# Kernel tuning notes

Hardware: AMD Instinct MI355X
Metric: run time of the kernel (lower is better)

Reference implementation:

```python
import jax, jax.numpy as jnp
import numpy as np

D_MODEL = 512
NUM_EXPERTS = 8
TOP_K = 2
FFN = 2048
H = 2 * D_MODEL            # GRU hidden per direction
GRU_OUT = 4 * D_MODEL      # bidirectional concat
B, T = 8, 1024
BAL_W, Z_W = 0.01, 0.001


def setup_inputs() -> dict:
    key = jax.random.key(0)
    ks = jax.random.split(key, 12)
    s = 1.0 / np.sqrt(H)  # torch GRU uniform init scale
    u = lambda k, shape: jax.random.uniform(k, shape, jnp.float32, -s, s)
    tn = lambda k, shape: jax.random.normal(k, shape, jnp.float32) * 0.02
    return {
        "x": jax.random.normal(ks[0], (B, T, D_MODEL), jnp.float32),
        # GRU params, stacked [2 directions, ...]; gate order (r, z, n) as in torch
        "gru_Wih": u(ks[1], (2, 3 * H, D_MODEL)),
        "gru_Whh": u(ks[2], (2, 3 * H, H)),
        "gru_bih": u(ks[3], (2, 3 * H)),
        "gru_bhh": u(ks[4], (2, 3 * H)),
        "gate_W": tn(ks[5], (NUM_EXPERTS, GRU_OUT)),
        "gate_b": jnp.zeros((NUM_EXPERTS,), jnp.float32),
        "W1": tn(ks[6], (NUM_EXPERTS, GRU_OUT, FFN)),
        "b1": jnp.zeros((NUM_EXPERTS, FFN), jnp.float32),
        "W2": tn(ks[7], (NUM_EXPERTS, FFN, D_MODEL)),
        "b2": jnp.zeros((NUM_EXPERTS, D_MODEL), jnp.float32),
    }


def _gru_bidir(x, Wih, Whh, bih, bhh):
    # x: [B,T,D]; returns [B,T,2H]
    Bn = x.shape[0]

    def run(d, reverse):
        # precompute input projections: [T,B,3H]
        xg = jnp.swapaxes(jnp.einsum('btd,gd->btg', x, Wih[d]) + bih[d], 0, 1)
        Whh_d, bhh_d = Whh[d], bhh[d]

        def step(h, xt):
            hg = h @ Whh_d.T + bhh_d
            xr, xz, xn = jnp.split(xt, 3, axis=-1)
            hr, hz, hn = jnp.split(hg, 3, axis=-1)
            r = jax.nn.sigmoid(xr + hr)
            z = jax.nn.sigmoid(xz + hz)
            n = jnp.tanh(xn + r * hn)
            h_new = (1.0 - z) * n + z * h
            return h_new, h_new

        h0 = jnp.zeros((Bn, H), x.dtype)
        _, ys = jax.lax.scan(step, h0, xg, reverse=reverse)  # ys[t] aligned with time t
        return jnp.swapaxes(ys, 0, 1)

    return jnp.concatenate([run(0, False), run(1, True)], axis=-1)


def reference(x, gru_Wih, gru_Whh, gru_bih, gru_bhh, gate_W, gate_b, W1, b1, W2, b2):
    Bn, Tn, _ = x.shape
    n = Bn * Tn
    E = NUM_EXPERTS

    gru_out = _gru_bidir(x, gru_Wih, gru_Whh, gru_bih, gru_bhh)
    gru_out = jax.nn.leaky_relu(gru_out, 0.01)          # dropout=0.0 -> identity
    flat = gru_out.reshape(n, GRU_OUT)

    # gating (expert_bias buffer is zeros at init)
    logits = flat @ gate_W.T + gate_b                    # [n,E]
    z_loss = Z_W * jnp.mean(jnp.square(jax.nn.logsumexp(logits, axis=-1)))
    scores = jax.nn.softmax(logits, axis=-1)
    top_scores, top_idx = jax.lax.top_k(scores, TOP_K)   # [n,K]
    weights = top_scores / jnp.sum(top_scores, axis=-1, keepdims=True)

    expert_mask = jnp.sum(jax.nn.one_hot(top_idx, E, dtype=jnp.float32), axis=1)  # [n,E]
    f = jax.lax.stop_gradient(jnp.mean(expert_mask, axis=0))
    P = jnp.mean(scores, axis=0)
    balance_loss = BAL_W * E * jnp.sum(f * P)
    aux_loss = balance_loss + z_loss

    # masked-dense expert combine (math identical to gather/scatter loop)
    output = jnp.zeros((n, D_MODEL), jnp.float32)
    for e in range(E):
        h = jax.nn.gelu(flat @ W1[e] + b1[e], approximate=False)  # [n,FFN]
        out_e = h @ W2[e] + b2[e]                                 # [n,D]
        w_e = jnp.sum(weights * (top_idx == e), axis=-1)          # [n]
        output = output + w_e[:, None] * out_e

    return output.reshape(Bn, Tn, D_MODEL).astype(x.dtype), aux_loss
```

## Files before the change

### kernel.cpp

```cpp
#include <hip/hip_runtime.h>
#include <math.h>

#define NTOK 8192
#define DM   512
#define HID  1024
#define G3H  3072
#define GOUT 2048
#define FFND 2048
#define NEXP 8

typedef float f32x4 __attribute__((ext_vector_type(4)));

#define XG_OFF    0ULL
#define HG_OFF    0ULL
#define OG_OFF    134217728ULL
#define FLAT_OFF  201326592ULL
#define HBUF_OFF  268435456ULL
#define FLAGS_OFF 268566528ULL
#define IMETA_OFF 268567552ULL
#define FMETA_OFF 268571648ULL
#define TKIDX_OFF 268575744ULL
#define TKW_OFF   268641280ULL
#define PAIRT_OFF 268706816ULL
#define PAIRW_OFF 268772352ULL
#define SLOT_OFF  268837888ULL

__global__ void k0_init(float* p) {
    int i = blockIdx.x * 256 + threadIdx.x;
    if (i < 35072) p[i] = 0.f;
}

__global__ __launch_bounds__(256, 2) void k1_sgemm_bt(
    const float* __restrict__ A, const float* __restrict__ B,
    const float* __restrict__ bias, float* __restrict__ C) {
    __shared__ float As[16 * 132];
    __shared__ float Bs[16 * 132];
    const int tid = threadIdx.x;
    const int m0 = blockIdx.y * 128;
    const int n0 = blockIdx.x * 128;
    const int tx = tid & 15, ty = tid >> 4;
    const int arow = tid >> 2, ac4 = (tid & 3) * 4;
    float acc[8][8];
#pragma unroll
    for (int i = 0; i < 8; ++i)
#pragma unroll
        for (int j = 0; j < 8; ++j) acc[i][j] = 0.f;

    for (int k0 = 0; k0 < 512; k0 += 16) {
        __syncthreads();
#pragma unroll
        for (int r = 0; r < 2; ++r) {
            int row = r * 64 + arow;
            float4 va = *(const float4*)(A + (size_t)(m0 + row) * 512 + k0 + ac4);
            As[(ac4 + 0) * 132 + row] = va.x;
            As[(ac4 + 1) * 132 + row] = va.y;
            As[(ac4 + 2) * 132 + row] = va.z;
            As[(ac4 + 3) * 132 + row] = va.w;
            float4 vb = *(const float4*)(B + (size_t)(n0 + row) * 512 + k0 + ac4);
            Bs[(ac4 + 0) * 132 + row] = vb.x;
            Bs[(ac4 + 1) * 132 + row] = vb.y;
            Bs[(ac4 + 2) * 132 + row] = vb.z;
            Bs[(ac4 + 3) * 132 + row] = vb.w;
        }
        __syncthreads();
#pragma unroll
        for (int k = 0; k < 16; ++k) {
            float4 a0 = *(const float4*)&As[k * 132 + ty * 8];
            float4 a1 = *(const float4*)&As[k * 132 + ty * 8 + 4];
            float4 b0 = *(const float4*)&Bs[k * 132 + tx * 8];
            float4 b1 = *(const float4*)&Bs[k * 132 + tx * 8 + 4];
            float av[8] = {a0.x, a0.y, a0.z, a0.w, a1.x, a1.y, a1.z, a1.w};
            float bv[8] = {b0.x, b0.y, b0.z, b0.w, b1.x, b1.y, b1.z, b1.w};
#pragma unroll
            for (int i = 0; i < 8; ++i)
#pragma unroll
                for (int j = 0; j < 8; ++j) acc[i][j] = fmaf(av[i], bv[j], acc[i][j]);
        }
    }
    float4 c0 = *(const float4*)(bias + n0 + tx * 8);
    float4 c1 = *(const float4*)(bias + n0 + tx * 8 + 4);
    float bb[8] = {c0.x, c0.y, c0.z, c0.w, c1.x, c1.y, c1.z, c1.w};
#pragma unroll
    for (int i = 0; i < 8; ++i) {
        float* op = C + (size_t)(m0 + ty * 8 + i) * 6144 + n0 + tx * 8;
        float4 o0 = make_float4(acc[i][0] + bb[0], acc[i][1] + bb[1],
                                acc[i][2] + bb[2], acc[i][3] + bb[3]);
        float4 o1 = make_float4(acc[i][4] + bb[4], acc[i][5] + bb[5],
                                acc[i][6] + bb[6], acc[i][7] + bb[7]);
        *(float4*)op = o0;
        *(float4*)(op + 4) = o1;
    }
}

__global__ __launch_bounds__(256) void k2_gru(
    const float* __restrict__ Whh, const float* __restrict__ bhh,
    const float* __restrict__ xg, float* __restrict__ flat,
    float* hbuf, int* flags) {
    __shared__ float hlsf[8192];
    __shared__ float red[64 * 196];
    __shared__ float s2b[192];
    char* hls = (char*)hlsf;
    const int tid = threadIdx.x;
    const int dir = blockIdx.x >> 7;
    const int wg = blockIdx.x & 127;
    const int j0 = wg << 3;
    float* hb = hbuf + dir * 16384;
    int* fl = flags + dir * 128;
    const int rg = tid >> 6;
    const int kc = tid & 63;
    const int swz = (kc & 7) << 4;
    const int lane = tid & 63;

    const float* W0 = Whh + (size_t)dir * G3H * HID;
    float wreg[6][16];
#pragma unroll
    for (int rr = 0; rr < 6; ++rr) {
        const int r = rg * 6 + rr;
        const float* wp = W0 + (size_t)(((r >> 3) << 10) + j0 + (r & 7)) * 1024 + (kc << 4);
        const float4 w0 = ((const float4*)wp)[0];
        const float4 w1 = ((const float4*)wp)[1];
        const float4 w2 = ((const float4*)wp)[2];
        const float4 w3 = ((const float4*)wp)[3];
        wreg[rr][0] = w0.x;  wreg[rr][1] = w0.y;  wreg[rr][2] = w0.z;  wreg[rr][3] = w0.w;
        wreg[rr][4] = w1.x;  wreg[rr][5] = w1.y;  wreg[rr][6] = w1.z;  wreg[rr][7] = w1.w;
        wreg[rr][8] = w2.x;  wreg[rr][9] = w2.y;  wreg[rr][10] = w2.z; wreg[rr][11] = w2.w;
        wreg[rr][12] = w3.x; wreg[rr][13] = w3.y; wreg[rr][14] = w3.z; wreg[rr][15] = w3.w;
    }
    float bhh_r = 0.f;
    if (tid < 192) {
        const int r = tid >> 3;
        bhh_r = bhh[dir * G3H + ((r >> 3) << 10) + j0 + (r & 7)];
    }
    const int u = tid >> 3, bb = tid & 7;
    const int wswz = ((tid >> 5) & 7) << 4;
    float hprev = 0.f;

    for (int s = 1; s <= 1024; ++s) {
        const int te = dir ? (1024 - s) : (s - 1);
        float xr = 0.f, xz = 0.f, xn = 0.f;
        if (tid < 64) {
            const float* xp = xg + (size_t)((bb << 10) + te) * 6144 + dir * G3H + j0 + u;
            xr = xp[0];
            xz = xp[1024];
            xn = xp[2048];
        }
        if (s > 1) {
            const int c0 = s - 1;
            int it = 0;
            for (;;) {
                int f0 = __hip_atomic_load(fl + lane, __ATOMIC_RELAXED, __HIP_MEMORY_SCOPE_AGENT);
                int f1 = __hip_atomic_load(fl + 64 + lane, __ATOMIC_RELAXED, __HIP_MEMORY_SCOPE_AGENT);
                if (__all((f0 >= c0) && (f1 >= c0))) break;
                if (++it > (1 << 22)) break;
                __builtin_amdgcn_s_sleep(1);
            }
        }
        asm volatile("" ::: "memory");
        const float* hp = hb + (((s - 1) & 1) << 13);
        const float* hbase = hp + (tid << 2);
        f32x4 hv4[8];
#pragma unroll
        for (int c = 0; c < 8; ++c)
            asm volatile("global_load_dwordx4 %0, %1, off sc0 sc1"
                         : "=v"(hv4[c]) : "v"(hbase + (c << 10)));
        asm volatile("s_waitcnt vmcnt(0)" ::: "memory");
        __builtin_amdgcn_sched_barrier(0);
#pragma unroll
        for (int c = 0; c < 8; ++c) {
            const int off = ((c << 12) + (tid << 4)) ^ wswz;
            *(f32x4*)(hls + off) = hv4[c];
        }
        __syncthreads();
        float acc[6][8];
#pragma unroll
        for (int rr = 0; rr < 6; ++rr)
#pragma unroll
            for (int q = 0; q < 8; ++q) acc[rr][q] = 0.f;
#pragma unroll
        for (int i = 0; i < 16; ++i) {
            const int kbase = ((kc << 4) + i) << 5;
            const float4 hA = *(const float4*)(hls + (kbase ^ swz));
            const float4 hB = *(const float4*)(hls + ((kbase + 16) ^ swz));
#pragma unroll
            for (int rr = 0; rr < 6; ++rr) {
                const float w = wreg[rr][i];
                acc[rr][0] = fmaf(w, hA.x, acc[rr][0]);
                acc[rr][1] = fmaf(w, hA.y, acc[rr][1]);
                acc[rr][2] = fmaf(w, hA.z, acc[rr][2]);
                acc[rr][3] = fmaf(w, hA.w, acc[rr][3]);
                acc[rr][4] = fmaf(w, hB.x, acc[rr][4]);
                acc[rr][5] = fmaf(w, hB.y, acc[rr][5]);
                acc[rr][6] = fmaf(w, hB.z, acc[rr][6]);
                acc[rr][7] = fmaf(w, hB.w, acc[rr][7]);
            }
        }
        float* rp = red + kc * 196 + rg * 48;
#pragma unroll
        for (int rr = 0; rr < 6; ++rr) {
            *(float4*)(rp + (rr << 3)) =
                make_float4(acc[rr][0], acc[rr][1], acc[rr][2], acc[rr][3]);
            *(float4*)(rp + (rr << 3) + 4) =
                make_float4(acc[rr][4], acc[rr][5], acc[rr][6], acc[rr][7]);
        }
        __syncthreads();
        if (tid < 192) {
            float a0 = 0.f, a1 = 0.f, a2 = 0.f, a3 = 0.f;
#pragma unroll
            for (int q = 0; q < 64; q += 4) {
                a0 += red[(q + 0) * 196 + tid];
                a1 += red[(q + 1) * 196 + tid];
                a2 += red[(q + 2) * 196 + tid];
                a3 += red[(q + 3) * 196 + tid];
            }
            s2b[tid] = (a0 + a1) + (a2 + a3) + bhh_r;
        }
        __syncthreads();
        if (tid < 64) {
            const float hr = s2b[tid];
            const float hz = s2b[64 + tid];
            const float hn = s2b[128 + tid];
            const float rg_ = 1.f / (1.f + expf(-(xr + hr)));
            const float zg_ = 1.f / (1.f + expf(-(xz + hz)));
            const float ng_ = tanhf(xn + rg_ * hn);
            const float hnew = (1.f - zg_) * ng_ + zg_ * hprev;
            hprev = hnew;
            __hip_atomic_store(hb + ((s & 1) << 13) + ((j0 + u) << 3) + bb, hnew,
                               __ATOMIC_RELAXED, __HIP_MEMORY_SCOPE_AGENT);
            __builtin_amdgcn_s_waitcnt(0);
            if (tid == 0)
                __hip_atomic_store(fl + wg, s, __ATOMIC_RELAXED, __HIP_MEMORY_SCOPE_AGENT);
            const float lr = hnew > 0.f ? hnew : 0.01f * hnew;
            flat[(size_t)((bb << 10) + te) * 2048 + dir * 1024 + j0 + u] = lr;
        }
    }
}

__global__ __launch_bounds__(256) void k3_gate(
    const float* __restrict__ flat, const float* __restrict__ gate_W,
    const float* __restrict__ gate_b,
    int* __restrict__ tk_idx, float* __restrict__ tk_w,
    int* __restrict__ counts, float* __restrict__ fmeta) {
    __shared__ float gw[8 * 2048];
    __shared__ float bP[9];
    __shared__ int bC[8];
    const int tid = threadIdx.x;
    for (int i = tid; i < 8 * 2048; i += 256) gw[i] = gate_W[i];
    if (tid < 9) bP[tid] = 0.f;
    if (tid < 8) bC[tid] = 0;
    __syncthreads();
    const int lane = tid & 63, w = tid >> 6;
    const int tbase = blockIdx.x * 16 + w * 4;
    for (int j = 0; j < 4; ++j) {
        int t = tbase + j;
        const float* fr = flat + (size_t)t * 2048;
        float a[8];
#pragma unroll
        for (int e = 0; e < 8; ++e) a[e] = 0.f;
        for (int i = 0; i < 32; ++i) {
            float v = fr[i * 64 + lane];
#pragma unroll
            for (int e = 0; e < 8; ++e) a[e] = fmaf(v, gw[e * 2048 + i * 64 + lane], a[e]);
        }
#pragma unroll
        for (int e = 0; e < 8; ++e) {
#pragma unroll
            for (int off = 32; off > 0; off >>= 1) a[e] += __shfl_down(a[e], off);
        }
        if (lane == 0) {
            float lg[8];
#pragma unroll
            for (int e = 0; e < 8; ++e) lg[e] = a[e] + gate_b[e];
            float m = lg[0];
#pragma unroll
            for (int e = 1; e < 8; ++e) m = fmaxf(m, lg[e]);
            float sc[8], ssum = 0.f;
#pragma unroll
            for (int e = 0; e < 8; ++e) { sc[e] = expf(lg[e] - m); ssum += sc[e]; }
            float inv = 1.f / ssum;
#pragma unroll
            for (int e = 0; e < 8; ++e) sc[e] *= inv;
            float lse = m + logf(ssum);
            int i1 = 0; float s1 = sc[0];
#pragma unroll
            for (int e = 1; e < 8; ++e) if (sc[e] > s1) { s1 = sc[e]; i1 = e; }
            int i2 = (i1 == 0) ? 1 : 0; float s2v = sc[i2];
#pragma unroll
            for (int e = 0; e < 8; ++e) if (e != i1 && sc[e] > s2v) { s2v = sc[e]; i2 = e; }
            float wsum = s1 + s2v;
            tk_idx[2 * t] = i1; tk_idx[2 * t + 1] = i2;
            tk_w[2 * t] = s1 / wsum; tk_w[2 * t + 1] = s2v / wsum;
            atomicAdd(&bC[i1], 1);
            atomicAdd(&bC[i2], 1);
#pragma unroll
            for (int e = 0; e < 8; ++e) atomicAdd(&bP[e], sc[e]);
            atomicAdd(&bP[8], lse * lse);
        }
    }
    __syncthreads();
    if (tid < 8) {
        atomicAdd(&counts[tid], bC[tid]);
        atomicAdd(&fmeta[tid], bP[tid]);
    }
    if (tid == 8) atomicAdd(&fmeta[8], bP[8]);
}

__global__ void k4_sched(int* im, float* fm, float* aux_out) {
    int tid = threadIdx.x;
    if (tid < 136) { im[32 + tid] = -1; im[168 + tid] = 0; }
    __syncthreads();
    if (tid == 0) {
        int off = 0;
        for (int e = 0; e < 8; ++e) { im[16 + e] = off; im[8 + e] = off; off += im[e]; }
        im[24] = off;
        int T = 0;
        for (int e = 0; e < 8; ++e) {
            int c = im[e], o = im[16 + e];
            for (int i = 0; i < c; i += 128) { im[32 + T] = e; im[168 + T] = o + i; ++T; }
        }
        im[25] = T;
        float fP = 0.f;
        for (int e = 0; e < 8; ++e) fP += ((float)im[e] / 8192.f) * (fm[e] / 8192.f);
        *aux_out = 0.01f * 8.f * fP + 0.001f * (fm[8] / 8192.f);
    }
}

__global__ __launch_bounds__(256) void k5_scatter(
    const int* __restrict__ tk_idx, const float* __restrict__ tk_w,
    int* __restrict__ im, int* __restrict__ pair_t,
    float* __restrict__ pair_w, int* __restrict__ slot) {
    __shared__ int cnt[8], base[8];
    const int tid = threadIdx.x;
    if (tid < 8) cnt[tid] = 0;
    __syncthreads();
    const int t = blockIdx.x * 256 + tid;
    const int e0 = tk_idx[2 * t], e1 = tk_idx[2 * t + 1];
    const int p0 = atomicAdd(&cnt[e0], 1);
    const int p1 = atomicAdd(&cnt[e1], 1);
    __syncthreads();
    if (tid < 8) base[tid] = atomicAdd(&im[8 + tid], cnt[tid]);
    __syncthreads();
    const int q0 = base[e0] + p0, q1 = base[e1] + p1;
    pair_t[q0] = t; pair_w[q0] = tk_w[2 * t];     slot[2 * t] = q0;
    pair_t[q1] = t; pair_w[q1] = tk_w[2 * t + 1]; slot[2 * t + 1] = q1;
}

__global__ __launch_bounds__(256, 2) void k6_ffn1(
    const float* __restrict__ flat, const float* __restrict__ W1,
    const float* __restrict__ b1, const int* __restrict__ im,
    const int* __restrict__ pair_t, float* __restrict__ Hg) {
    const int rt = blockIdx.x % 136;
    const int nt = blockIdx.x / 136;
    const int e = im[32 + rt];
    if (e < 0) return;
    const int pStart = im[168 + rt];
    const int pEnd = im[16 + e + 1];
    __shared__ float As[16 * 132];
    __shared__ float Bs[16 * 132];
    const int tid = threadIdx.x;
    const int tx = tid & 15, ty = tid >> 4;
    const int n0 = nt * 128;
    const float* Bb = W1 + (size_t)e * 2048 * 2048;
    const int arow = tid >> 2, ac4 = (tid & 3) * 4;
    const int bk = tid >> 4, bn = (tid & 15) * 8;
    int r0 = pStart + arow;       if (r0 > pEnd - 1) r0 = pEnd - 1;
    int r1 = pStart + 64 + arow;  if (r1 > pEnd - 1) r1 = pEnd - 1;
    const float* arp0 = flat + (size_t)pair_t[r0] * 2048;
    const float* arp1 = flat + (size_t)pair_t[r1] * 2048;
    float acc[8][8];
#pragma unroll
    for (int i = 0; i < 8; ++i)
#pragma unroll
        for (int j = 0; j < 8; ++j) acc[i][j] = 0.f;

    for (int k0 = 0; k0 < 2048; k0 += 16) {
        __syncthreads();
        {
            float4 va = *(const float4*)(arp0 + k0 + ac4);
            As[(ac4 + 0) * 132 + arow] = va.x;
            As[(ac4 + 1) * 132 + arow] = va.y;
            As[(ac4 + 2) * 132 + arow] = va.z;
            As[(ac4 + 3) * 132 + arow] = va.w;
            float4 vb = *(const float4*)(arp1 + k0 + ac4);
            As[(ac4 + 0) * 132 + 64 + arow] = vb.x;
            As[(ac4 + 1) * 132 + 64 + arow] = vb.y;
            As[(ac4 + 2) * 132 + 64 + arow] = vb.z;
            As[(ac4 + 3) * 132 + 64 + arow] = vb.w;
            float4 w0 = *(const float4*)(Bb + (size_t)(k0 + bk) * 2048 + n0 + bn);
            float4 w1 = *(const float4*)(Bb + (size_t)(k0 + bk) * 2048 + n0 + bn + 4);
            *(float4*)&Bs[bk * 132 + bn] = w0;
            *(float4*)&Bs[bk * 132 + bn + 4] = w1;
        }
        __syncthreads();
#pragma unroll
        for (int k = 0; k < 16; ++k) {
            float4 a0 = *(const float4*)&As[k * 132 + ty * 8];
            float4 a1 = *(const float4*)&As[k * 132 + ty * 8 + 4];
            float4 b0 = *(const float4*)&Bs[k * 132 + tx * 8];
            float4 b1v = *(const float4*)&Bs[k * 132 + tx * 8 + 4];
            float av[8] = {a0.x, a0.y, a0.z, a0.w, a1.x, a1.y, a1.z, a1.w};
            float bv[8] = {b0.x, b0.y, b0.z, b0.w, b1v.x, b1v.y, b1v.z, b1v.w};
#pragma unroll
            for (int i = 0; i < 8; ++i)
#pragma unroll
                for (int j = 0; j < 8; ++j) acc[i][j] = fmaf(av[i], bv[j], acc[i][j]);
        }
    }
    float4 c0 = *(const float4*)(b1 + (size_t)e * 2048 + n0 + tx * 8);
    float4 c1 = *(const float4*)(b1 + (size_t)e * 2048 + n0 + tx * 8 + 4);
    float bb[8] = {c0.x, c0.y, c0.z, c0.w, c1.x, c1.y, c1.z, c1.w};
#pragma unroll
    for (int i = 0; i < 8; ++i) {
        int p = pStart + ty * 8 + i;
        if (p < pEnd) {
            float* op = Hg + (size_t)p * 2048 + n0 + tx * 8;
            float o[8];
#pragma unroll
            for (int j = 0; j < 8; ++j) {
                float xv = acc[i][j] + bb[j];
                o[j] = 0.5f * xv * (1.f + erff(xv * 0.70710678118654752f));
            }
            *(float4*)op = make_float4(o[0], o[1], o[2], o[3]);
            *(float4*)(op + 4) = make_float4(o[4], o[5], o[6], o[7]);
        }
    }
}

__global__ __launch_bounds__(256, 2) void k7_ffn2(
    const float* __restrict__ Hg, const float* __restrict__ W2,
    const float* __restrict__ b2, const int* __restrict__ im,
    float* __restrict__ Og) {
    const int rt = blockIdx.x % 136;
    const int nt = blockIdx.x / 136;
    const int e = im[32 + rt];
    if (e < 0) return;
    const int pStart = im[168 + rt];
    const int pEnd = im[16 + e + 1];
    __shared__ float As[16 * 132];
    __shared__ float Bs[16 * 132];
    const int tid = threadIdx.x;
    const int tx = tid & 15, ty = tid >> 4;
    const int n0 = nt * 128;
    const float* Bb = W2 + (size_t)e * 2048 * 512;
    const int arow = tid >> 2, ac4 = (tid & 3) * 4;
    const int bk = tid >> 4, bn = (tid & 15) * 8;
    int r0 = pStart + arow;       if (r0 > pEnd - 1) r0 = pEnd - 1;
    int r1 = pStart + 64 + arow;  if (r1 > pEnd - 1) r1 = pEnd - 1;
    const float* arp0 = Hg + (size_t)r0 * 2048;
    const float* arp1 = Hg + (size_t)r1 * 2048;
    float acc[8][8];
#pragma unroll
    for (int i = 0; i < 8; ++i)
#pragma unroll
        for (int j = 0; j < 8; ++j) acc[i][j] = 0.f;

    for (int k0 = 0; k0 < 2048; k0 += 16) {
        __syncthreads();
        {
            float4 va = *(const float4*)(arp0 + k0 + ac4);
            As[(ac4 + 0) * 132 + arow] = va.x;
            As[(ac4 + 1) * 132 + arow] = va.y;
            As[(ac4 + 2) * 132 + arow] = va.z;
            As[(ac4 + 3) * 132 + arow] = va.w;
            float4 vb = *(const float4*)(arp1 + k0 + ac4);
            As[(ac4 + 0) * 132 + 64 + arow] = vb.x;
            As[(ac4 + 1) * 132 + 64 + arow] = vb.y;
            As[(ac4 + 2) * 132 + 64 + arow] = vb.z;
            As[(ac4 + 3) * 132 + 64 + arow] = vb.w;
            float4 w0 = *(const float4*)(Bb + (size_t)(k0 + bk) * 512 + n0 + bn);
            float4 w1 = *(const float4*)(Bb + (size_t)(k0 + bk) * 512 + n0 + bn + 4);
            *(float4*)&Bs[bk * 132 + bn] = w0;
            *(float4*)&Bs[bk * 132 + bn + 4] = w1;
        }
        __syncthreads();
#pragma unroll
        for (int k = 0; k < 16; ++k) {
            float4 a0 = *(const float4*)&As[k * 132 + ty * 8];
            float4 a1 = *(const float4*)&As[k * 132 + ty * 8 + 4];
            float4 b0 = *(const float4*)&Bs[k * 132 + tx * 8];
            float4 b1v = *(const float4*)&Bs[k * 132 + tx * 8 + 4];
            float av[8] = {a0.x, a0.y, a0.z, a0.w, a1.x, a1.y, a1.z, a1.w};
            float bv[8] = {b0.x, b0.y, b0.z, b0.w, b1v.x, b1v.y, b1v.z, b1v.w};
#pragma unroll
            for (int i = 0; i < 8; ++i)
#pragma unroll
                for (int j = 0; j < 8; ++j) acc[i][j] = fmaf(av[i], bv[j], acc[i][j]);
        }
    }
    float4 c0 = *(const float4*)(b2 + (size_t)e * 512 + n0 + tx * 8);
    float4 c1 = *(const float4*)(b2 + (size_t)e * 512 + n0 + tx * 8 + 4);
    float bb[8] = {c0.x, c0.y, c0.z, c0.w, c1.x, c1.y, c1.z, c1.w};
#pragma unroll
    for (int i = 0; i < 8; ++i) {
        int p = pStart + ty * 8 + i;
        if (p < pEnd) {
            float* op = Og + (size_t)p * 512 + n0 + tx * 8;
            *(float4*)op = make_float4(acc[i][0] + bb[0], acc[i][1] + bb[1],
                                       acc[i][2] + bb[2], acc[i][3] + bb[3]);
            *(float4*)(op + 4) = make_float4(acc[i][4] + bb[4], acc[i][5] + bb[5],
                                             acc[i][6] + bb[6], acc[i][7] + bb[7]);
        }
    }
}

__global__ __launch_bounds__(256) void k8_comb(
    const float* __restrict__ Og, const int* __restrict__ slot,
    const float* __restrict__ pw, float* __restrict__ out) {
    const int i4 = blockIdx.x * 256 + threadIdx.x;
    const int t = i4 >> 7;
    const int d = (i4 & 127) << 2;
    const int s0 = slot[2 * t], s1 = slot[2 * t + 1];
    const float w0 = pw[s0], w1 = pw[s1];
    float4 a = *(const float4*)(Og + (size_t)s0 * 512 + d);
    float4 b = *(const float4*)(Og + (size_t)s1 * 512 + d);
    float4 o = make_float4(w0 * a.x + w1 * b.x, w0 * a.y + w1 * b.y,
                           w0 * a.z + w1 * b.z, w0 * a.w + w1 * b.w);
    *(float4*)(out + (size_t)t * 512 + d) = o;
}

extern "C" void kernel_launch(void* const* d_in, const int* in_sizes, int n_in,
                              void* d_out, int out_size, void* d_ws, size_t ws_size,
                              hipStream_t stream) {
    (void)in_sizes; (void)n_in; (void)out_size; (void)ws_size;
    const float* x   = (const float*)d_in[0];
    const float* Wih = (const float*)d_in[1];
    const float* Whh = (const float*)d_in[2];
    const float* bih = (const float*)d_in[3];
    const float* bhh = (const float*)d_in[4];
    const float* gW  = (const float*)d_in[5];
    const float* gb  = (const float*)d_in[6];
    const float* W1  = (const float*)d_in[7];
    const float* b1  = (const float*)d_in[8];
    const float* W2  = (const float*)d_in[9];
    const float* b2  = (const float*)d_in[10];
    float* out = (float*)d_out;
    char* ws = (char*)d_ws;
    float* xg    = (float*)(ws + XG_OFF);
    float* Hg    = (float*)(ws + HG_OFF);
    float* Og    = (float*)(ws + OG_OFF);
    float* flat  = (float*)(ws + FLAT_OFF);
    float* hbuf  = (float*)(ws + HBUF_OFF);
    int*   flags = (int*)(ws + FLAGS_OFF);
    int*   im    = (int*)(ws + IMETA_OFF);
    float* fm    = (float*)(ws + FMETA_OFF);
    int*   tki   = (int*)(ws + TKIDX_OFF);
    float* tkw   = (float*)(ws + TKW_OFF);
    int*   prt   = (int*)(ws + PAIRT_OFF);
    float* prw   = (float*)(ws + PAIRW_OFF);
    int*   slt   = (int*)(ws + SLOT_OFF);

    hipLaunchKernelGGL(k0_init, dim3(138), dim3(256), 0, stream, (float*)(ws + HBUF_OFF));
    hipLaunchKernelGGL(k1_sgemm_bt, dim3(48, 64), dim3(256), 0, stream, x, Wih, bih, xg);
    hipLaunchKernelGGL(k2_gru, dim3(256), dim3(256), 0, stream, Whh, bhh, xg, flat, hbuf, flags);
    hipLaunchKernelGGL(k3_gate, dim3(512), dim3(256), 0, stream, flat, gW, gb, tki, tkw, im, fm);
    hipLaunchKernelGGL(k4_sched, dim3(1), dim3(256), 0, stream, im, fm, out + 4194304);
    hipLaunchKernelGGL(k5_scatter, dim3(32), dim3(256), 0, stream, tki, tkw, im, prt, prw, slt);
    hipLaunchKernelGGL(k6_ffn1, dim3(136 * 16), dim3(256), 0, stream, flat, W1, b1, im, prt, Hg);
    hipLaunchKernelGGL(k7_ffn2, dim3(136 * 4), dim3(256), 0, stream, Hg, W2, b2, im, Og);
    hipLaunchKernelGGL(k8_comb, dim3(4096), dim3(256), 0, stream, Og, slt, prw, out);
}
```

Baseline: 10.86 ms.

## Embed step parity bit in GRU hidden state to replace flag synchronization

After: 9.558 ms. -12.0%, faster.

```diff
diff --git a/kernel.cpp b/kernel.cpp
--- a/kernel.cpp
+++ b/kernel.cpp
@@ -25,9 +25,10 @@
 #define PAIRW_OFF 268772352ULL
 #define SLOT_OFF  268837888ULL
 
-__global__ void k0_init(float* p) {
+__global__ void k0_init(unsigned* p) {
     int i = blockIdx.x * 256 + threadIdx.x;
-    if (i < 35072) p[i] = 0.f;
+    if (i < 32768) p[i] = (unsigned)((i >> 13) & 1);
+    else if (i < 35072) p[i] = 0u;
 }
 
 __global__ __launch_bounds__(256, 2) void k1_sgemm_bt(
@@ -95,7 +96,7 @@
 __global__ __launch_bounds__(256) void k2_gru(
     const float* __restrict__ Whh, const float* __restrict__ bhh,
     const float* __restrict__ xg, float* __restrict__ flat,
-    float* hbuf, int* flags) {
+    float* hbuf) {
     __shared__ float hlsf[8192];
     __shared__ float red[64 * 196];
     __shared__ float s2b[192];
@@ -105,7 +106,6 @@
     const int wg = blockIdx.x & 127;
     const int j0 = wg << 3;
     float* hb = hbuf + dir * 16384;
-    int* fl = flags + dir * 128;
     const int rg = tid >> 6;
     const int kc = tid & 63;
     const int swz = (kc & 7) << 4;
@@ -144,27 +144,45 @@
             xz = xp[1024];
             xn = xp[2048];
         }
+        const float* hp = hb + (((s - 1) & 1) << 13);
+        const unsigned expb = (((unsigned)(s - 1)) >> 1) & 1u;
         if (s > 1) {
-            const int c0 = s - 1;
             int it = 0;
             for (;;) {
-                int f0 = __hip_atomic_load(fl + lane, __ATOMIC_RELAXED, __HIP_MEMORY_SCOPE_AGENT);
-                int f1 = __hip_atomic_load(fl + 64 + lane, __ATOMIC_RELAXED, __HIP_MEMORY_SCOPE_AGENT);
-                if (__all((f0 >= c0) && (f1 >= c0))) break;
+                float a = __hip_atomic_load(hp + (lane << 6) + 17,
+                                            __ATOMIC_RELAXED, __HIP_MEMORY_SCOPE_AGENT);
+                float b = __hip_atomic_load(hp + 4096 + (lane << 6) + 17,
+                                            __ATOMIC_RELAXED, __HIP_MEMORY_SCOPE_AGENT);
+                bool ok = ((__float_as_uint(a) & 1u) == expb) &&
+                          ((__float_as_uint(b) & 1u) == expb);
+                if (__all(ok)) break;
                 if (++it > (1 << 22)) break;
                 __builtin_amdgcn_s_sleep(1);
             }
         }
-        asm volatile("" ::: "memory");
-        const float* hp = hb + (((s - 1) & 1) << 13);
         const float* hbase = hp + (tid << 2);
         f32x4 hv4[8];
-#pragma unroll
-        for (int c = 0; c < 8; ++c)
-            asm volatile("global_load_dwordx4 %0, %1, off sc0 sc1"
-                         : "=v"(hv4[c]) : "v"(hbase + (c << 10)));
-        asm volatile("s_waitcnt vmcnt(0)" ::: "memory");
-        __builtin_amdgcn_sched_barrier(0);
+        {
+            int it2 = 0;
+            for (;;) {
+#pragma unroll
+                for (int c = 0; c < 8; ++c)
+                    asm volatile("global_load_dwordx4 %0, %1, off sc0 sc1"
+                                 : "=v"(hv4[c]) : "v"(hbase + (c << 10)));
+                asm volatile("s_waitcnt vmcnt(0)" ::: "memory");
+                __builtin_amdgcn_sched_barrier(0);
+                bool ok = true;
+#pragma unroll
+                for (int c = 0; c < 8; ++c) {
+                    ok = ok && ((__float_as_uint(hv4[c].x) & 1u) == expb)
+                            && ((__float_as_uint(hv4[c].y) & 1u) == expb)
+                            && ((__float_as_uint(hv4[c].z) & 1u) == expb)
+                            && ((__float_as_uint(hv4[c].w) & 1u) == expb);
+                }
+                if (__all(ok)) break;
+                if (++it2 > (1 << 18)) break;
+            }
+        }
 #pragma unroll
         for (int c = 0; c < 8; ++c) {
             const int off = ((c << 12) + (tid << 4)) ^ wswz;
@@ -224,11 +242,10 @@
             const float ng_ = tanhf(xn + rg_ * hn);
             const float hnew = (1.f - zg_) * ng_ + zg_ * hprev;
             hprev = hnew;
-            __hip_atomic_store(hb + ((s & 1) << 13) + ((j0 + u) << 3) + bb, hnew,
+            const unsigned hu = (__float_as_uint(hnew) & ~1u) | (((unsigned)s >> 1) & 1u);
+            __hip_atomic_store(hb + ((s & 1) << 13) + ((j0 + u) << 3) + bb,
+                               __uint_as_float(hu),
                                __ATOMIC_RELAXED, __HIP_MEMORY_SCOPE_AGENT);
-            __builtin_amdgcn_s_waitcnt(0);
-            if (tid == 0)
-                __hip_atomic_store(fl + wg, s, __ATOMIC_RELAXED, __HIP_MEMORY_SCOPE_AGENT);
             const float lr = hnew > 0.f ? hnew : 0.01f * hnew;
             flat[(size_t)((bb << 10) + te) * 2048 + dir * 1024 + j0 + u] = lr;
         }
@@ -539,7 +556,6 @@
     float* Og    = (float*)(ws + OG_OFF);
     float* flat  = (float*)(ws + FLAT_OFF);
     float* hbuf  = (float*)(ws + HBUF_OFF);
-    int*   flags = (int*)(ws + FLAGS_OFF);
     int*   im    = (int*)(ws + IMETA_OFF);
     float* fm    = (float*)(ws + FMETA_OFF);
     int*   tki   = (int*)(ws + TKIDX_OFF);
@@ -548,9 +564,9 @@
     float* prw   = (float*)(ws + PAIRW_OFF);
     int*   slt   = (int*)(ws + SLOT_OFF);
 
-    hipLaunchKernelGGL(k0_init, dim3(138), dim3(256), 0, stream, (float*)(ws + HBUF_OFF));
+    hipLaunchKernelGGL(k0_init, dim3(138), dim3(256), 0, stream, (unsigned*)(ws + HBUF_OFF));
     hipLaunchKernelGGL(k1_sgemm_bt, dim3(48, 64), dim3(256), 0, stream, x, Wih, bih, xg);
-    hipLaunchKernelGGL(k2_gru, dim3(256), dim3(256), 0, stream, Whh, bhh, xg, flat, hbuf, flags);
+    hipLaunchKernelGGL(k2_gru, dim3(256), dim3(256), 0, stream, Whh, bhh, xg, flat, hbuf);
     hipLaunchKernelGGL(k3_gate, dim3(512), dim3(256), 0, stream, flat, gW, gb, tki, tkw, im, fm);
     hipLaunchKernelGGL(k4_sched, dim3(1), dim3(256), 0, stream, im, fm, out + 4194304);
     hipLaunchKernelGGL(k5_scatter, dim3(32), dim3(256), 0, stream, tki, tkw, im, prt, prw, slt);
```
